# Performance work log

Hardware: AMD Instinct MI355X
Metric: run time of the kernel (lower is better)

## Reference

```python
import jax, jax.numpy as jnp
import numpy as np


def feature_map(x):
    # phi(x) = elu(x) + 1 (ensures positivity)
    return jax.nn.elu(x) + 1.0


def setup_inputs() -> dict:
    key = jax.random.key(0)
    k0, k1, k2, k3 = jax.random.split(key, 4)
    B, T, d_model, D = 4, 4096, 1024, 128
    x = jax.random.normal(k0, (B, T, d_model), dtype=jnp.float32)
    s = 1.0 / np.sqrt(d_model)
    Wq = jax.random.normal(k1, (d_model, D), dtype=jnp.float32) * s
    Wk = jax.random.normal(k2, (d_model, D), dtype=jnp.float32) * s
    Wv = jax.random.normal(k3, (d_model, D), dtype=jnp.float32) * s
    return {"x": x, "Wq": Wq, "Wk": Wk, "Wv": Wv}


def _causal_linear_attention(phi_q, phi_k, v):
    # phi_q, phi_k: [B,T,D]; v: [B,T,Dv]
    B, T, D = phi_q.shape
    Dv = v.shape[-1]
    # time-major for scan: [T,B,D]
    qT = jnp.swapaxes(phi_q, 0, 1)
    kT = jnp.swapaxes(phi_k, 0, 1)
    vT = jnp.swapaxes(v, 0, 1)

    def step(carry, inp):
        kv, ks = carry                       # kv: [B,D,Dv], ks: [B,D]
        qt, kt, vt = inp                     # each [B,D] / [B,Dv]
        kv = kv + kt[:, :, None] * vt[:, None, :]   # k_t^T v_t outer product
        ks = ks + kt
        num = jnp.einsum('bd,bdv->bv', qt, kv)      # [B,Dv]
        den = jnp.einsum('bd,bd->b', qt, ks)[:, None]
        return (kv, ks), num / den

    init = (jnp.zeros((B, D, Dv), phi_q.dtype), jnp.zeros((B, D), phi_q.dtype))
    _, outT = jax.lax.scan(step, init, (qT, kT, vT))  # outT: [T,B,Dv]
    return jnp.swapaxes(outT, 0, 1)


def reference(x, Wq, Wk, Wv):
    q = x @ Wq
    k = x @ Wk
    v = x @ Wv
    phi_q = feature_map(q)
    phi_k = feature_map(k)
    # dropout is identity in eval mode
    return _causal_linear_attention(phi_q, phi_k, v)
```

## Files before the change

kernel.cpp:

```cpp
#include <hip/hip_runtime.h>

#define DMODEL 1024
#define DHEAD 128
#define CHUNK 128
#define NCHUNK 32

typedef __attribute__((ext_vector_type(4))) float f32x4;
typedef __attribute__((ext_vector_type(8))) short bf16x8;

__device__ __forceinline__ unsigned short f2bf(float f) {
  union { float f; unsigned u; } v; v.f = f;
  unsigned r = v.u + 0x7FFF + ((v.u >> 16) & 1);
  return (unsigned short)(r >> 16);
}
__device__ __forceinline__ float bf2f(unsigned short h) {
  union { unsigned u; float f; } v; v.u = ((unsigned)h) << 16;
  return v.f;
}
__device__ __forceinline__ unsigned cvtpk(float lo, float hi) {
  unsigned r;
  asm("v_cvt_pk_bf16_f32 %0, %1, %2" : "=v"(r) : "v"(lo), "v"(hi));
  return r;
}
__device__ __forceinline__ void gload16(const void* g, void* l) {
  __builtin_amdgcn_global_load_lds(
      (const __attribute__((address_space(1))) unsigned int*)g,
      (__attribute__((address_space(3))) unsigned int*)l, 16, 0, 0);
}

__global__ __launch_bounds__(256) void transpose_w_kernel(
    const float* __restrict__ Wq, const float* __restrict__ Wk,
    const float* __restrict__ Wv, unsigned short* __restrict__ WT) {
  int id = blockIdx.x * 256 + threadIdx.x;
  int w = id >> 17;
  int rem = id & 131071;
  int n = rem >> 10;
  int k = rem & 1023;
  const float* W = (w == 0) ? Wq : (w == 1) ? Wk : Wv;
  WT[id] = f2bf(W[(size_t)k * DHEAD + n]);
}

__global__ __launch_bounds__(256) void proj_kernel(
    const float* __restrict__ x, const unsigned short* __restrict__ WT,
    unsigned short* __restrict__ phiQ, unsigned short* __restrict__ phiK,
    unsigned short* __restrict__ Vb) {
  const int m0 = blockIdx.x * 64;
  const int n0 = blockIdx.y * 64;

  __shared__ float xs[64][64];
  __shared__ unsigned short wl[3][64][64];

  const int tid = threadIdx.x;
  const int wave = tid >> 6;
  const int lane = tid & 63;
  const int lrow = lane & 15, kgrp = lane >> 4;

  f32x4 acc[3][4];
#pragma unroll
  for (int w3 = 0; w3 < 3; ++w3)
#pragma unroll
    for (int j = 0; j < 4; ++j) acc[w3][j] = (f32x4)0.0f;

  for (int kk = 0; kk < DMODEL; kk += 64) {
    if (kk) __syncthreads();
#pragma unroll
    for (int i = 0; i < 4; ++i) {
      int instr = i * 4 + wave;
      int row = instr * 4 + (lane >> 4);
      int slot = lane & 15;
      int gcol = (slot ^ (row & 7)) << 2;
      gload16(&x[(size_t)(m0 + row) * DMODEL + kk + gcol],
              (char*)xs + instr * 1024);
    }
#pragma unroll
    for (int i = 0; i < 6; ++i) {
      int j = i * 4 + wave;
      int w3 = j >> 3;
      int jj = j & 7;
      int row = jj * 8 + (lane >> 3);
      int slot = lane & 7;
      int gcol = (slot ^ (row & 7)) << 3;
      gload16(&WT[(size_t)w3 * (DHEAD * DMODEL) + (size_t)(n0 + row) * DMODEL + kk + gcol],
              (char*)wl + w3 * 8192 + jj * 1024);
    }
    __syncthreads();

#pragma unroll
    for (int ks2 = 0; ks2 < 2; ++ks2) {
      int arow = wave * 16 + lrow;
      int s0 = ks2 * 8 + kgrp * 2;
      const float4 f0 = *reinterpret_cast<const float4*>(
          &xs[arow][(s0 ^ (arow & 7)) << 2]);
      const float4 f1 = *reinterpret_cast<const float4*>(
          &xs[arow][((s0 + 1) ^ (arow & 7)) << 2]);
      union { unsigned u[4]; bf16x8 v; } p;
      p.u[0] = cvtpk(f0.x, f0.y);
      p.u[1] = cvtpk(f0.z, f0.w);
      p.u[2] = cvtpk(f1.x, f1.y);
      p.u[3] = cvtpk(f1.z, f1.w);
      bf16x8 af = p.v;
#pragma unroll
      for (int w3 = 0; w3 < 3; ++w3)
#pragma unroll
        for (int nt = 0; nt < 4; ++nt) {
          int brow = nt * 16 + lrow;
          int bs = ks2 * 4 + kgrp;
          bf16x8 bf = *reinterpret_cast<const bf16x8*>(
              &wl[w3][brow][(bs ^ (brow & 7)) << 3]);
          acc[w3][nt] = __builtin_amdgcn_mfma_f32_16x16x32_bf16(af, bf, acc[w3][nt], 0, 0, 0);
        }
    }
  }
#pragma unroll
  for (int w3 = 0; w3 < 3; ++w3) {
    unsigned short* outp = (w3 == 0) ? phiQ : (w3 == 1) ? phiK : Vb;
#pragma unroll
    for (int nt = 0; nt < 4; ++nt)
#pragma unroll
      for (int r = 0; r < 4; ++r) {
        int row = m0 + wave * 16 + kgrp * 4 + r;
        int col = n0 + nt * 16 + lrow;
        float v = acc[w3][nt][r];
        if (w3 < 2) v = (v > 0.0f) ? (v + 1.0f) : __expf(v);
        outp[(size_t)row * DHEAD + col] = f2bf(v);
      }
  }
}

__global__ __launch_bounds__(256) void chunkkv_kernel(
    const unsigned short* __restrict__ phiK, const unsigned short* __restrict__ Vb,
    float* __restrict__ KVc, float* __restrict__ ksc) {
  const size_t base = (size_t)blockIdx.x * CHUNK * DHEAD;
  __shared__ unsigned short kt[128][136];
  __shared__ unsigned short vt[128][136];
  __shared__ float csum[2][128];
  const int tid = threadIdx.x;
  const int wave = tid >> 6, lane = tid & 63;
  const int lrow = lane & 15, kgrp = lane >> 4;

  {
    int t = tid & 127, dp = tid >> 7;
#pragma unroll
    for (int i = 0; i < 8; ++i) {
      int d0 = (dp + 2 * i) * 8;
      uint4 k4 = *reinterpret_cast<const uint4*>(&phiK[base + (size_t)t * DHEAD + d0]);
      uint4 v4 = *reinterpret_cast<const uint4*>(&Vb[base + (size_t)t * DHEAD + d0]);
      const unsigned short* kp = reinterpret_cast<const unsigned short*>(&k4);
      const unsigned short* vp = reinterpret_cast<const unsigned short*>(&v4);
#pragma unroll
      for (int j = 0; j < 8; ++j) { kt[d0 + j][t] = kp[j]; vt[d0 + j][t] = vp[j]; }
    }
  }
  __syncthreads();

  f32x4 acc[2][8];
#pragma unroll
  for (int i = 0; i < 2; ++i)
#pragma unroll
    for (int j = 0; j < 8; ++j) acc[i][j] = (f32x4)0.0f;
#pragma unroll
  for (int ks = 0; ks < 4; ++ks) {
    int t0 = ks * 32 + kgrp * 8;
    bf16x8 afrag[2];
#pragma unroll
    for (int tr = 0; tr < 2; ++tr)
      afrag[tr] = *reinterpret_cast<const bf16x8*>(&vt[wave * 32 + tr * 16 + lrow][t0]);
#pragma unroll
    for (int tc = 0; tc < 8; ++tc) {
      bf16x8 bfrag = *reinterpret_cast<const bf16x8*>(&kt[tc * 16 + lrow][t0]);
      acc[0][tc] = __builtin_amdgcn_mfma_f32_16x16x32_bf16(afrag[0], bfrag, acc[0][tc], 0, 0, 0);
      acc[1][tc] = __builtin_amdgcn_mfma_f32_16x16x32_bf16(afrag[1], bfrag, acc[1][tc], 0, 0, 0);
    }
  }
  float* KVout = KVc + (size_t)blockIdx.x * (DHEAD * DHEAD);
#pragma unroll
  for (int tr = 0; tr < 2; ++tr)
#pragma unroll
    for (int tc = 0; tc < 8; ++tc)
#pragma unroll
      for (int r = 0; r < 4; ++r) {
        int dv = wave * 32 + tr * 16 + kgrp * 4 + r;
        int d = tc * 16 + lrow;
        KVout[dv * DHEAD + d] = acc[tr][tc][r];
      }
  {
    int d = tid & 127, hh = tid >> 7;
    float s = 0.0f;
    for (int t = hh * 64; t < hh * 64 + 64; ++t) s += bf2f(kt[d][t]);
    csum[hh][d] = s;
  }
  __syncthreads();
  if (tid < 128) ksc[(size_t)blockIdx.x * DHEAD + tid] = csum[0][tid] + csum[1][tid];
}

__global__ __launch_bounds__(256) void prefix_kernel(
    const float* __restrict__ KVc, const float* __restrict__ ksc,
    unsigned short* __restrict__ KVp, float* __restrict__ ksp) {
  if (blockIdx.x < 256) {
    int id = blockIdx.x * 256 + threadIdx.x;
    int b = id >> 14;
    int e = id & 16383;
    size_t base = (size_t)b * NCHUNK * 16384 + e;
    float acc = 0.0f;
    for (int c = 0; c < NCHUNK; ++c) {
      KVp[base + (size_t)c * 16384] = f2bf(acc);
      acc += KVc[base + (size_t)c * 16384];
    }
  } else {
    for (int i = threadIdx.x; i < 512; i += 256) {
      int b = i >> 7, d = i & 127;
      size_t base = (size_t)b * NCHUNK * DHEAD + d;
      float acc = 0.0f;
      for (int c = 0; c < NCHUNK; ++c) {
        ksp[base + (size_t)c * DHEAD] = acc;
        acc += ksc[base + (size_t)c * DHEAD];
      }
    }
  }
}

__global__ __launch_bounds__(256) void out_kernel(
    const unsigned short* __restrict__ phiQ, const unsigned short* __restrict__ phiK,
    const unsigned short* __restrict__ Vb, const unsigned short* __restrict__ KVp,
    const float* __restrict__ ksp, float* __restrict__ outp) {
  const int c = blockIdx.x;
  const int h = blockIdx.y;
  const size_t kvbase = (size_t)c * CHUNK * DHEAD;
  const size_t qbase = kvbase + (size_t)h * 64 * DHEAD;
  __shared__ unsigned short qb[64][136];
  __shared__ unsigned short kb[128][136];
  __shared__ unsigned short vt[128][136];
  __shared__ float dsum[4][64];
  __shared__ float ks_l[128];
  const int tid = threadIdx.x;
  const int wave = tid >> 6, lane = tid & 63;
  const int lrow = lane & 15, kgrp = lane >> 4;

#pragma unroll
  for (int it = 0; it < 4; ++it) {
    int idx = it * 256 + tid;
    int t = idx >> 4;
    int d0 = (idx & 15) << 3;
    *reinterpret_cast<uint4*>(&qb[t][d0]) =
        *reinterpret_cast<const uint4*>(&phiQ[qbase + (size_t)t * DHEAD + d0]);
  }
  if (tid < 128) ks_l[tid] = ksp[(size_t)c * DHEAD + tid];
  if (h == 0) {
#pragma unroll
    for (int it = 0; it < 4; ++it) {
      int idx = it * 256 + tid;
      int t = idx >> 4;
      int d0 = (idx & 15) << 3;
      *reinterpret_cast<uint4*>(&kb[t][d0]) =
          *reinterpret_cast<const uint4*>(&phiK[kvbase + (size_t)t * DHEAD + d0]);
    }
    int t = tid & 63, dp = tid >> 6;
#pragma unroll
    for (int i = 0; i < 4; ++i) {
      int d0 = (dp + 4 * i) * 8;
      uint4 v4 = *reinterpret_cast<const uint4*>(&Vb[kvbase + (size_t)t * DHEAD + d0]);
      const unsigned short* vp = reinterpret_cast<const unsigned short*>(&v4);
#pragma unroll
      for (int j = 0; j < 8; ++j) vt[d0 + j][t] = vp[j];
    }
  } else {
#pragma unroll
    for (int it = 0; it < 8; ++it) {
      int idx = it * 256 + tid;
      int t = idx >> 4;
      int d0 = (idx & 15) << 3;
      *reinterpret_cast<uint4*>(&kb[t][d0]) =
          *reinterpret_cast<const uint4*>(&phiK[kvbase + (size_t)t * DHEAD + d0]);
    }
    int t = tid & 127, dp = tid >> 7;
#pragma unroll
    for (int i = 0; i < 8; ++i) {
      int d0 = (dp + 2 * i) * 8;
      uint4 v4 = *reinterpret_cast<const uint4*>(&Vb[kvbase + (size_t)t * DHEAD + d0]);
      const unsigned short* vp = reinterpret_cast<const unsigned short*>(&v4);
#pragma unroll
      for (int j = 0; j < 8; ++j) vt[d0 + j][t] = vp[j];
    }
  }
  __syncthreads();

  if (h == 0) {
    f32x4 sa[4];
#pragma unroll
    for (int i = 0; i < 4; ++i) sa[i] = (f32x4)0.0f;
#pragma unroll
    for (int ks = 0; ks < 4; ++ks) {
      int d0 = ks * 32 + kgrp * 8;
      bf16x8 af = *reinterpret_cast<const bf16x8*>(&qb[wave * 16 + lrow][d0]);
#pragma unroll
      for (int tc = 0; tc < 4; ++tc) {
        bf16x8 bf = *reinterpret_cast<const bf16x8*>(&kb[tc * 16 + lrow][d0]);
        sa[tc] = __builtin_amdgcn_mfma_f32_16x16x32_bf16(af, bf, sa[tc], 0, 0, 0);
      }
    }
    __syncthreads();
#pragma unroll
    for (int tc = 0; tc < 4; ++tc)
#pragma unroll
      for (int r = 0; r < 4; ++r) {
        int trow = wave * 16 + kgrp * 4 + r;
        int s = tc * 16 + lrow;
        kb[trow][s] = f2bf((s <= trow) ? sa[tc][r] : 0.0f);
      }
  } else {
    f32x4 sa[8];
#pragma unroll
    for (int i = 0; i < 8; ++i) sa[i] = (f32x4)0.0f;
#pragma unroll
    for (int ks = 0; ks < 4; ++ks) {
      int d0 = ks * 32 + kgrp * 8;
      bf16x8 af = *reinterpret_cast<const bf16x8*>(&qb[wave * 16 + lrow][d0]);
#pragma unroll
      for (int tc = 0; tc < 8; ++tc) {
        bf16x8 bf = *reinterpret_cast<const bf16x8*>(&kb[tc * 16 + lrow][d0]);
        sa[tc] = __builtin_amdgcn_mfma_f32_16x16x32_bf16(af, bf, sa[tc], 0, 0, 0);
      }
    }
    __syncthreads();
#pragma unroll
    for (int tc = 0; tc < 8; ++tc)
#pragma unroll
      for (int r = 0; r < 4; ++r) {
        int trow = wave * 16 + kgrp * 4 + r;
        int s = tc * 16 + lrow;
        kb[trow][s] = f2bf((s <= 64 + trow) ? sa[tc][r] : 0.0f);
      }
  }
  __syncthreads();

  {
    int t = tid & 63, h4 = tid >> 6;
    float s = 0.0f;
    if (h4 < 2) {
      if (h4 == 0 || h == 1) {
        for (int j = h4 * 64; j < h4 * 64 + 64; ++j) s += bf2f(kb[t][j]);
      }
    } else {
      for (int j = (h4 - 2) * 64; j < (h4 - 2) * 64 + 64; ++j)
        s += bf2f(qb[t][j]) * ks_l[j];
    }
    dsum[h4][t] = s;
  }

  f32x4 acc[8];
#pragma unroll
  for (int i = 0; i < 8; ++i) acc[i] = (f32x4)0.0f;
  {
    const int nks = (h == 0) ? 2 : 4;
    for (int ks = 0; ks < nks; ++ks) {
      int t0 = ks * 32 + kgrp * 8;
      bf16x8 af = *reinterpret_cast<const bf16x8*>(&kb[wave * 16 + lrow][t0]);
#pragma unroll
      for (int tc = 0; tc < 8; ++tc) {
        bf16x8 bf = *reinterpret_cast<const bf16x8*>(&vt[tc * 16 + lrow][t0]);
        acc[tc] = __builtin_amdgcn_mfma_f32_16x16x32_bf16(af, bf, acc[tc], 0, 0, 0);
      }
    }
  }
  __syncthreads();

#pragma unroll
  for (int it = 0; it < 8; ++it) {
    int idx = it * 256 + tid;
    int dv = idx >> 4;
    int d0 = (idx & 15) << 3;
    *reinterpret_cast<uint4*>(&vt[dv][d0]) =
        *reinterpret_cast<const uint4*>(&KVp[(size_t)c * 16384 + (size_t)dv * DHEAD + d0]);
  }
  __syncthreads();

#pragma unroll
  for (int ks = 0; ks < 4; ++ks) {
    int d0 = ks * 32 + kgrp * 8;
    bf16x8 af = *reinterpret_cast<const bf16x8*>(&qb[wave * 16 + lrow][d0]);
#pragma unroll
    for (int tc = 0; tc < 8; ++tc) {
      bf16x8 bf = *reinterpret_cast<const bf16x8*>(&vt[tc * 16 + lrow][d0]);
      acc[tc] = __builtin_amdgcn_mfma_f32_16x16x32_bf16(af, bf, acc[tc], 0, 0, 0);
    }
  }

#pragma unroll
  for (int tc = 0; tc < 8; ++tc)
#pragma unroll
    for (int r = 0; r < 4; ++r) {
      int trow = wave * 16 + kgrp * 4 + r;
      int dv = tc * 16 + lrow;
      float den = dsum[0][trow] + dsum[1][trow] + dsum[2][trow] + dsum[3][trow];
      outp[qbase + (size_t)trow * DHEAD + dv] = acc[tc][r] / den;
    }
}

extern "C" void kernel_launch(void* const* d_in, const int* in_sizes, int n_in,
                              void* d_out, int out_size, void* d_ws, size_t ws_size,
                              hipStream_t stream) {
  const float* x  = (const float*)d_in[0];
  const float* Wq = (const float*)d_in[1];
  const float* Wk = (const float*)d_in[2];
  const float* Wv = (const float*)d_in[3];
  float* out = (float*)d_out;
  char* ws = (char*)d_ws;
  unsigned short* phiQ = (unsigned short*)(ws + 0);
  unsigned short* phiK = (unsigned short*)(ws + 4194304);
  unsigned short* Vb   = (unsigned short*)(ws + 8388608);
  unsigned short* WT   = (unsigned short*)(ws + 12582912);
  float*          KVc  = (float*)(ws + 13369344);
  unsigned short* KVp  = (unsigned short*)(ws + 21757952);
  float*          ksc  = (float*)(ws + 25952256);
  float*          ksp  = (float*)(ws + 26017792);

  transpose_w_kernel<<<1536, 256, 0, stream>>>(Wq, Wk, Wv, WT);
  proj_kernel<<<dim3(256, 2), 256, 0, stream>>>(x, WT, phiQ, phiK, Vb);
  chunkkv_kernel<<<128, 256, 0, stream>>>(phiK, Vb, KVc, ksc);
  prefix_kernel<<<257, 256, 0, stream>>>(KVc, ksc, KVp, ksp);
  out_kernel<<<dim3(128, 2), 256, 0, stream>>>(phiQ, phiK, Vb, KVp, ksp, out);
}
```

Measured before the change: 57.65 us.

## Shrink projection tiles with XCD-aware mapping and split chunk KV over Dv

```diff
diff --git a/kernel.cpp b/kernel.cpp
--- a/kernel.cpp
+++ b/kernel.cpp
@@ -44,10 +44,13 @@
     const float* __restrict__ x, const unsigned short* __restrict__ WT,
     unsigned short* __restrict__ phiQ, unsigned short* __restrict__ phiK,
     unsigned short* __restrict__ Vb) {
-  const int m0 = blockIdx.x * 64;
-  const int n0 = blockIdx.y * 64;
-
-  __shared__ float xs[64][64];
+  const int bid = blockIdx.x;
+  const int xcd = bid & 7;
+  const int slot = bid >> 3;
+  const int n0 = (slot & 1) << 6;
+  const int m0 = ((xcd << 6) | (slot >> 1)) << 5;
+
+  __shared__ float xs[32][64];
   __shared__ unsigned short wl[3][64][64];
 
   const int tid = threadIdx.x;
@@ -55,20 +58,20 @@
   const int lane = tid & 63;
   const int lrow = lane & 15, kgrp = lane >> 4;
 
-  f32x4 acc[3][4];
+  f32x4 acc[3][2];
 #pragma unroll
   for (int w3 = 0; w3 < 3; ++w3)
 #pragma unroll
-    for (int j = 0; j < 4; ++j) acc[w3][j] = (f32x4)0.0f;
+    for (int mi = 0; mi < 2; ++mi) acc[w3][mi] = (f32x4)0.0f;
 
   for (int kk = 0; kk < DMODEL; kk += 64) {
     if (kk) __syncthreads();
 #pragma unroll
-    for (int i = 0; i < 4; ++i) {
+    for (int i = 0; i < 2; ++i) {
       int instr = i * 4 + wave;
       int row = instr * 4 + (lane >> 4);
-      int slot = lane & 15;
-      int gcol = (slot ^ (row & 7)) << 2;
+      int slotc = lane & 15;
+      int gcol = (slotc ^ (row & 7)) << 2;
       gload16(&x[(size_t)(m0 + row) * DMODEL + kk + gcol],
               (char*)xs + instr * 1024);
     }
@@ -78,8 +81,8 @@
       int w3 = j >> 3;
       int jj = j & 7;
       int row = jj * 8 + (lane >> 3);
-      int slot = lane & 7;
-      int gcol = (slot ^ (row & 7)) << 3;
+      int slotc = lane & 7;
+      int gcol = (slotc ^ (row & 7)) << 3;
       gload16(&WT[(size_t)w3 * (DHEAD * DMODEL) + (size_t)(n0 + row) * DMODEL + kk + gcol],
               (char*)wl + w3 * 8192 + jj * 1024);
     }
@@ -87,40 +90,44 @@
 
 #pragma unroll
     for (int ks2 = 0; ks2 < 2; ++ks2) {
-      int arow = wave * 16 + lrow;
-      int s0 = ks2 * 8 + kgrp * 2;
-      const float4 f0 = *reinterpret_cast<const float4*>(
-          &xs[arow][(s0 ^ (arow & 7)) << 2]);
-      const float4 f1 = *reinterpret_cast<const float4*>(
-          &xs[arow][((s0 + 1) ^ (arow & 7)) << 2]);
-      union { unsigned u[4]; bf16x8 v; } p;
-      p.u[0] = cvtpk(f0.x, f0.y);
-      p.u[1] = cvtpk(f0.z, f0.w);
-      p.u[2] = cvtpk(f1.x, f1.y);
-      p.u[3] = cvtpk(f1.z, f1.w);
-      bf16x8 af = p.v;
-#pragma unroll
-      for (int w3 = 0; w3 < 3; ++w3)
-#pragma unroll
-        for (int nt = 0; nt < 4; ++nt) {
-          int brow = nt * 16 + lrow;
-          int bs = ks2 * 4 + kgrp;
-          bf16x8 bf = *reinterpret_cast<const bf16x8*>(
-              &wl[w3][brow][(bs ^ (brow & 7)) << 3]);
-          acc[w3][nt] = __builtin_amdgcn_mfma_f32_16x16x32_bf16(af, bf, acc[w3][nt], 0, 0, 0);
-        }
+      bf16x8 af[2];
+#pragma unroll
+      for (int mi = 0; mi < 2; ++mi) {
+        int arow = mi * 16 + lrow;
+        int s0 = ks2 * 8 + kgrp * 2;
+        const float4 f0 = *reinterpret_cast<const float4*>(
+            &xs[arow][(s0 ^ (arow & 7)) << 2]);
+        const float4 f1 = *reinterpret_cast<const float4*>(
+            &xs[arow][((s0 + 1) ^ (arow & 7)) << 2]);
+        union { unsigned u[4]; bf16x8 v; } p;
+        p.u[0] = cvtpk(f0.x, f0.y);
+        p.u[1] = cvtpk(f0.z, f0.w);
+        p.u[2] = cvtpk(f1.x, f1.y);
+        p.u[3] = cvtpk(f1.z, f1.w);
+        af[mi] = p.v;
+      }
+#pragma unroll
+      for (int w3 = 0; w3 < 3; ++w3) {
+        int brow = wave * 16 + lrow;
+        int bs = ks2 * 4 + kgrp;
+        bf16x8 bf = *reinterpret_cast<const bf16x8*>(
+            &wl[w3][brow][(bs ^ (brow & 7)) << 3]);
+#pragma unroll
+        for (int mi = 0; mi < 2; ++mi)
+          acc[w3][mi] = __builtin_amdgcn_mfma_f32_16x16x32_bf16(af[mi], bf, acc[w3][mi], 0, 0, 0);
+      }
     }
   }
 #pragma unroll
   for (int w3 = 0; w3 < 3; ++w3) {
     unsigned short* outp = (w3 == 0) ? phiQ : (w3 == 1) ? phiK : Vb;
 #pragma unroll
-    for (int nt = 0; nt < 4; ++nt)
+    for (int mi = 0; mi < 2; ++mi)
 #pragma unroll
       for (int r = 0; r < 4; ++r) {
-        int row = m0 + wave * 16 + kgrp * 4 + r;
-        int col = n0 + nt * 16 + lrow;
-        float v = acc[w3][nt][r];
+        int row = m0 + mi * 16 + kgrp * 4 + r;
+        int col = n0 + wave * 16 + lrow;
+        float v = acc[w3][mi][r];
         if (w3 < 2) v = (v > 0.0f) ? (v + 1.0f) : __expf(v);
         outp[(size_t)row * DHEAD + col] = f2bf(v);
       }
@@ -130,9 +137,11 @@
 __global__ __launch_bounds__(256) void chunkkv_kernel(
     const unsigned short* __restrict__ phiK, const unsigned short* __restrict__ Vb,
     float* __restrict__ KVc, float* __restrict__ ksc) {
-  const size_t base = (size_t)blockIdx.x * CHUNK * DHEAD;
+  const int c = blockIdx.x;
+  const int yv = blockIdx.y;
+  const size_t base = (size_t)c * CHUNK * DHEAD;
   __shared__ unsigned short kt[128][136];
-  __shared__ unsigned short vt[128][136];
+  __shared__ unsigned short vt[64][136];
   __shared__ float csum[2][128];
   const int tid = threadIdx.x;
   const int wave = tid >> 6, lane = tid & 63;
@@ -144,53 +153,52 @@
     for (int i = 0; i < 8; ++i) {
       int d0 = (dp + 2 * i) * 8;
       uint4 k4 = *reinterpret_cast<const uint4*>(&phiK[base + (size_t)t * DHEAD + d0]);
-      uint4 v4 = *reinterpret_cast<const uint4*>(&Vb[base + (size_t)t * DHEAD + d0]);
       const unsigned short* kp = reinterpret_cast<const unsigned short*>(&k4);
+#pragma unroll
+      for (int j = 0; j < 8; ++j) kt[d0 + j][t] = kp[j];
+    }
+#pragma unroll
+    for (int i = 0; i < 4; ++i) {
+      int dl = (dp + 2 * i) * 8;
+      uint4 v4 = *reinterpret_cast<const uint4*>(
+          &Vb[base + (size_t)t * DHEAD + yv * 64 + dl]);
       const unsigned short* vp = reinterpret_cast<const unsigned short*>(&v4);
 #pragma unroll
-      for (int j = 0; j < 8; ++j) { kt[d0 + j][t] = kp[j]; vt[d0 + j][t] = vp[j]; }
+      for (int j = 0; j < 8; ++j) vt[dl + j][t] = vp[j];
     }
   }
   __syncthreads();
 
-  f32x4 acc[2][8];
-#pragma unroll
-  for (int i = 0; i < 2; ++i)
-#pragma unroll
-    for (int j = 0; j < 8; ++j) acc[i][j] = (f32x4)0.0f;
+  f32x4 acc[8];
+#pragma unroll
+  for (int j = 0; j < 8; ++j) acc[j] = (f32x4)0.0f;
 #pragma unroll
   for (int ks = 0; ks < 4; ++ks) {
     int t0 = ks * 32 + kgrp * 8;
-    bf16x8 afrag[2];
-#pragma unroll
-    for (int tr = 0; tr < 2; ++tr)
-      afrag[tr] = *reinterpret_cast<const bf16x8*>(&vt[wave * 32 + tr * 16 + lrow][t0]);
+    bf16x8 afrag = *reinterpret_cast<const bf16x8*>(&vt[wave * 16 + lrow][t0]);
 #pragma unroll
     for (int tc = 0; tc < 8; ++tc) {
       bf16x8 bfrag = *reinterpret_cast<const bf16x8*>(&kt[tc * 16 + lrow][t0]);
-      acc[0][tc] = __builtin_amdgcn_mfma_f32_16x16x32_bf16(afrag[0], bfrag, acc[0][tc], 0, 0, 0);
-      acc[1][tc] = __builtin_amdgcn_mfma_f32_16x16x32_bf16(afrag[1], bfrag, acc[1][tc], 0, 0, 0);
-    }
-  }
-  float* KVout = KVc + (size_t)blockIdx.x * (DHEAD * DHEAD);
-#pragma unroll
-  for (int tr = 0; tr < 2; ++tr)
-#pragma unroll
-    for (int tc = 0; tc < 8; ++tc)
-#pragma unroll
-      for (int r = 0; r < 4; ++r) {
-        int dv = wave * 32 + tr * 16 + kgrp * 4 + r;
-        int d = tc * 16 + lrow;
-        KVout[dv * DHEAD + d] = acc[tr][tc][r];
-      }
-  {
+      acc[tc] = __builtin_amdgcn_mfma_f32_16x16x32_bf16(afrag, bfrag, acc[tc], 0, 0, 0);
+    }
+  }
+  float* KVout = KVc + (size_t)c * (DHEAD * DHEAD);
+#pragma unroll
+  for (int tc = 0; tc < 8; ++tc)
+#pragma unroll
+    for (int r = 0; r < 4; ++r) {
+      int dv = yv * 64 + wave * 16 + kgrp * 4 + r;
+      int d = tc * 16 + lrow;
+      KVout[dv * DHEAD + d] = acc[tc][r];
+    }
+  if (yv == 0) {
     int d = tid & 127, hh = tid >> 7;
     float s = 0.0f;
     for (int t = hh * 64; t < hh * 64 + 64; ++t) s += bf2f(kt[d][t]);
     csum[hh][d] = s;
-  }
-  __syncthreads();
-  if (tid < 128) ksc[(size_t)blockIdx.x * DHEAD + tid] = csum[0][tid] + csum[1][tid];
+    __syncthreads();
+    if (tid < 128) ksc[(size_t)c * DHEAD + tid] = csum[0][tid] + csum[1][tid];
+  }
 }
 
 __global__ __launch_bounds__(256) void prefix_kernel(
@@ -415,8 +423,8 @@
   float*          ksp  = (float*)(ws + 26017792);
 
   transpose_w_kernel<<<1536, 256, 0, stream>>>(Wq, Wk, Wv, WT);
-  proj_kernel<<<dim3(256, 2), 256, 0, stream>>>(x, WT, phiQ, phiK, Vb);
-  chunkkv_kernel<<<128, 256, 0, stream>>>(phiK, Vb, KVc, ksc);
+  proj_kernel<<<1024, 256, 0, stream>>>(x, WT, phiQ, phiK, Vb);
+  chunkkv_kernel<<<dim3(128, 2), 256, 0, stream>>>(phiK, Vb, KVc, ksc);
   prefix_kernel<<<257, 256, 0, stream>>>(KVc, ksc, KVp, ksp);
   out_kernel<<<dim3(128, 2), 256, 0, stream>>>(phiQ, phiK, Vb, KVp, ksp, out);
 }
```

Result: faster. 55.55 us (-3.6%).
